# Kernel tuning notes

Hardware: AMD Instinct MI355X
Metric: run time of the kernel (lower is better)

## Reference

```python
import jax, jax.numpy as jnp
import numpy as np

B, S, D = 2, 2048, 1024
H = 16
HD = D // H  # head_dim = 64


def setup_inputs() -> dict:
    key = jax.random.key(0)
    ks = jax.random.split(key, 6)
    scale = 0.02
    x = jax.random.normal(ks[0], (B, S, D), dtype=jnp.float32)
    Wq = jax.random.normal(ks[1], (D, D), dtype=jnp.float32) * scale
    Wk = jax.random.normal(ks[2], (D, D), dtype=jnp.float32) * scale
    Wv = jax.random.normal(ks[3], (D, D), dtype=jnp.float32) * scale
    Wo = jax.random.normal(ks[4], (D, D), dtype=jnp.float32) * scale
    bo = jax.random.normal(ks[5], (D,), dtype=jnp.float32) * scale
    return {"x": x, "Wq": Wq, "Wk": Wk, "Wv": Wv, "Wo": Wo, "bo": bo}


def reference(x, Wq, Wk, Wv, Wo, bo):
    b, s, d = x.shape
    # QKV projections (no bias, qkv_bias=False)
    Q = (x @ Wq).reshape(b, s, H, HD)
    K = (x @ Wk).reshape(b, s, H, HD)
    V = (x @ Wv).reshape(b, s, H, HD)
    # [b, h, q, k] attention scores
    scores = jnp.einsum('bqhd,bkhd->bhqk', Q, K)
    # causal mask: positions k > q masked to -inf (applied before scaling, as in source;
    # -inf / sqrt(hd) is still -inf so this matches)
    causal = jnp.triu(jnp.ones((s, s), dtype=bool), k=1)
    scores = jnp.where(causal, -jnp.inf, scores)
    att = jax.nn.softmax(scores / jnp.sqrt(jnp.float32(HD)), axis=-1)
    # dropout p=0.0 -> identity
    ctx = jnp.einsum('bhqk,bkhd->bqhd', att, V).reshape(b, s, d)
    return ctx @ Wo + bo
```

## Files before the change

### kernel.cpp

```cpp
#include <hip/hip_runtime.h>

typedef __bf16 bf16;
typedef __attribute__((ext_vector_type(8))) __bf16 bf16x8;
typedef __attribute__((ext_vector_type(4))) __bf16 bf16x4;
typedef __attribute__((ext_vector_type(4))) float floatx4;

#define MFMA16(a, b, c) __builtin_amdgcn_mfma_f32_16x16x32_bf16((a), (b), (c), 0, 0, 0)

static constexpr int BB = 2, SS = 2048, DD = 1024, HH = 16;
static constexpr int MM = BB * SS;
static constexpr int N_QKV = 3 * DD;

__device__ __forceinline__ float exp2c(float x) {
#if __has_builtin(__builtin_amdgcn_exp2f)
    return __builtin_amdgcn_exp2f(x);
#else
    return exp2f(x);
#endif
}

__device__ __forceinline__ void async16(const void* g, void* l) {
    __builtin_amdgcn_global_load_lds(
        (const __attribute__((address_space(1))) unsigned int*)g,
        (__attribute__((address_space(3))) unsigned int*)l, 16, 0, 0);
}

__global__ __launch_bounds__(256) void prep_kernel(const float* __restrict__ x,
                                                   bf16* __restrict__ xb,
                                                   const float* __restrict__ w0,
                                                   const float* __restrict__ w1,
                                                   const float* __restrict__ w2,
                                                   const float* __restrict__ w3,
                                                   bf16* __restrict__ outT) {
    const int blk = blockIdx.x, tid = threadIdx.x;
    if (blk < 4096) {
        int i = blk * 1024 + tid * 4;
        float4 v = *(const float4*)(x + i);
        bf16x4 o;
        o[0] = (bf16)v.x; o[1] = (bf16)v.y; o[2] = (bf16)v.z; o[3] = (bf16)v.w;
        *(bf16x4*)(xb + i) = o;
    } else {
        __shared__ float tile[32][33];
        const int wblk = blk - 4096;
        const int z = wblk >> 10, rem = wblk & 1023;
        const int by = rem >> 5, bx = rem & 31;
        const float* src = (z == 0) ? w0 : (z == 1) ? w1 : (z == 2) ? w2 : w3;
        bf16* dst = outT + (size_t)z * DD * DD;
        const int y0 = by * 32, x0 = bx * 32;
        {
            const int tx = tid & 7, ty = tid >> 3;
            float4 v = *(const float4*)(src + (size_t)(y0 + ty) * DD + x0 + tx * 4);
            tile[ty][tx * 4 + 0] = v.x;
            tile[ty][tx * 4 + 1] = v.y;
            tile[ty][tx * 4 + 2] = v.z;
            tile[ty][tx * 4 + 3] = v.w;
        }
        __syncthreads();
        {
            const int tx = tid & 7, c = tid >> 3;
            bf16x4 o;
            o[0] = (bf16)tile[tx * 4 + 0][c];
            o[1] = (bf16)tile[tx * 4 + 1][c];
            o[2] = (bf16)tile[tx * 4 + 2][c];
            o[3] = (bf16)tile[tx * 4 + 3][c];
            *(bf16x4*)(dst + (size_t)(x0 + c) * DD + y0 + tx * 4) = o;
        }
    }
}

template <int BM, int BN, bool OUT_BF16>
__global__ __launch_bounds__(256) void gemm_kernel(const bf16* __restrict__ A,
                                                   const bf16* __restrict__ Bt,
                                                   void* __restrict__ C,
                                                   const float* __restrict__ bias,
                                                   int K, int ldc) {
    constexpr int MT = BM / 32, NT = BN / 32;
    __shared__ bf16 As[BM * 64];
    __shared__ bf16 Bs[BN * 64];
    const int tid = threadIdx.x, wave = tid >> 6, lane = tid & 63;
    const int quad = lane >> 4, l16 = lane & 15;
    const int wm = wave >> 1, wn = wave & 1;
    const int m0 = blockIdx.y * BM, n0 = blockIdx.x * BN;
    const int l8r = lane >> 3, l8c = lane & 7;
    const int gch = ((l8c ^ l8r) * 8);

    floatx4 acc[MT][NT] = {};

    for (int k0 = 0; k0 < K; k0 += 64) {
        __syncthreads();
#pragma unroll
        for (int c = 0; c < BM / 32; ++c) {
            int r = wave * (BM / 4) + c * 8;
            async16(A + (size_t)(m0 + r + l8r) * K + k0 + gch, &As[r * 64]);
        }
#pragma unroll
        for (int c = 0; c < BN / 32; ++c) {
            int r = wave * (BN / 4) + c * 8;
            async16(Bt + (size_t)(n0 + r + l8r) * K + k0 + gch, &Bs[r * 64]);
        }
        __syncthreads();
#pragma unroll
        for (int cc = 0; cc < 2; ++cc) {
            bf16x8 af[MT], bv[NT];
#pragma unroll
            for (int i = 0; i < MT; ++i) {
                int row = wm * (BM / 2) + i * 16 + l16;
                af[i] = *(const bf16x8*)&As[row * 64 + ((cc * 4 + quad) ^ (row & 7)) * 8];
            }
#pragma unroll
            for (int j = 0; j < NT; ++j) {
                int row = wn * (BN / 2) + j * 16 + l16;
                bv[j] = *(const bf16x8*)&Bs[row * 64 + ((cc * 4 + quad) ^ (row & 7)) * 8];
            }
#pragma unroll
            for (int i = 0; i < MT; ++i)
#pragma unroll
                for (int j = 0; j < NT; ++j)
                    acc[i][j] = MFMA16(af[i], bv[j], acc[i][j]);
        }
    }

#pragma unroll
    for (int i = 0; i < MT; ++i)
#pragma unroll
        for (int j = 0; j < NT; ++j)
#pragma unroll
            for (int r = 0; r < 4; ++r) {
                int row = m0 + wm * (BM / 2) + i * 16 + quad * 4 + r;
                int col = n0 + wn * (BN / 2) + j * 16 + l16;
                if (OUT_BF16)
                    ((bf16*)C)[(size_t)row * ldc + col] = (bf16)acc[i][j][r];
                else
                    ((float*)C)[(size_t)row * ldc + col] = acc[i][j][r] + bias[col];
            }
}

__global__ __launch_bounds__(512, 2) void gemm192_kernel(const bf16* __restrict__ A,
                                                         const bf16* __restrict__ Bt,
                                                         bf16* __restrict__ C,
                                                         bf16* __restrict__ Vt_g,
                                                         int K, int ldc) {
    __shared__ __align__(16) bf16 As[2 * 256 * 64];
    __shared__ __align__(16) bf16 Bs[2 * 192 * 64];
    const int tid = threadIdx.x, wave = tid >> 6, lane = tid & 63;
    const int quad = lane >> 4, l16 = lane & 15;
    const int wm = wave >> 2, wn = wave & 3;
    const int m0 = blockIdx.y * 256, n0 = blockIdx.x * 192;
    const int l8r = lane >> 3, l8c = lane & 7;
    const int gch = (l8c ^ l8r) * 8;
    const int nk = K >> 6;

    floatx4 acc[2][4][3] = {};
    bf16x8 af[4][2], bn[3][2];

#define VMW(N) asm volatile("s_waitcnt vmcnt(" #N ")" ::: "memory")
#define BARX __builtin_amdgcn_s_barrier()

#define STAGE_A(H, KN, BUF)                                                       \
    {                                                                             \
        _Pragma("unroll") for (int c = 0; c < 2; ++c) {                           \
            int r0 = (H) * 128 + c * 64 + wave * 8;                               \
            async16(A + (size_t)(m0 + r0 + l8r) * K + (KN) + gch,                 \
                    &As[(BUF) * 16384 + r0 * 64]);                                \
        }                                                                         \
    }
#define STAGE_B(KN, BUF)                                                          \
    {                                                                             \
        _Pragma("unroll") for (int c = 0; c < 3; ++c) {                           \
            int r0 = wave * 24 + c * 8;                                           \
            async16(Bt + (size_t)(n0 + r0 + l8r) * K + (KN) + gch,                \
                    &Bs[(BUF) * 12288 + r0 * 64]);                                \
        }                                                                         \
    }
#define READ_A(MH, BUF)                                                           \
    {                                                                             \
        _Pragma("unroll") for (int m = 0; m < 4; ++m) {                           \
            int row = (MH) * 128 + wm * 64 + m * 16 + l16;                        \
            _Pragma("unroll") for (int kk = 0; kk < 2; ++kk)                      \
                af[m][kk] = *(const bf16x8*)&As[(BUF) * 16384 + row * 64 +        \
                                               (((kk * 4 + quad) ^ (row & 7)) * 8)]; \
        }                                                                         \
    }
#define READ_B(BUF)                                                               \
    {                                                                             \
        _Pragma("unroll") for (int n = 0; n < 3; ++n) {                           \
            int row = wn * 48 + n * 16 + l16;                                     \
            _Pragma("unroll") for (int kk = 0; kk < 2; ++kk)                      \
                bn[n][kk] = *(const bf16x8*)&Bs[(BUF) * 12288 + row * 64 +        \
                                               (((kk * 4 + quad) ^ (row & 7)) * 8)]; \
        }                                                                         \
    }
#define MMAC(MH)                                                                  \
    {                                                                             \
        __builtin_amdgcn_s_setprio(1);                                            \
        _Pragma("unroll") for (int m = 0; m < 4; ++m)                             \
            _Pragma("unroll") for (int n = 0; n < 3; ++n)                         \
                _Pragma("unroll") for (int kk = 0; kk < 2; ++kk)                  \
                    acc[MH][m][n] = MFMA16(af[m][kk], bn[n][kk], acc[MH][m][n]);  \
        __builtin_amdgcn_s_setprio(0);                                            \
    }

    STAGE_A(0, 0, 0);
    STAGE_B(0, 0);
    STAGE_A(1, 0, 0);

    for (int kt = 0; kt < nk; ++kt) {
        const int buf = kt & 1;
        const int knext = (kt + 1) << 6;
        const bool last = (kt == nk - 1);

        VMW(2);
        BARX;
        READ_A(0, buf);
        READ_B(buf);
        if (!last) { STAGE_A(0, knext, buf ^ 1); STAGE_B(knext, buf ^ 1); }
        MMAC(0);

        if (!last) { VMW(5); } else { VMW(0); }
        BARX;
        READ_A(1, buf);
        if (!last) STAGE_A(1, knext, buf ^ 1);
        MMAC(1);
    }

#undef VMW
#undef BARX
#undef STAGE_A
#undef STAGE_B
#undef READ_A
#undef READ_B
#undef MMAC

#pragma unroll
    for (int mh = 0; mh < 2; ++mh)
#pragma unroll
        for (int m = 0; m < 4; ++m)
#pragma unroll
            for (int n = 0; n < 3; ++n) {
                int grow = m0 + mh * 128 + wm * 64 + m * 16 + quad * 4;
                int gcol0 = n0 + wn * 48 + n * 16;
                if (gcol0 >= 2048) {
                    int bb = grow >> 11, s = grow & (SS - 1);
                    int vcol = gcol0 + l16 - 2048;
                    int hh = vcol >> 6, hd = vcol & 63;
                    bf16x4 pk;
#pragma unroll
                    for (int r = 0; r < 4; ++r) pk[r] = (bf16)acc[mh][m][n][r];
                    *(bf16x4*)&Vt_g[(((size_t)(bb * 16 + hh)) * 64 + hd) * SS + s] = pk;
                } else {
#pragma unroll
                    for (int r = 0; r < 4; ++r)
                        C[(size_t)(grow + r) * ldc + gcol0 + l16] = (bf16)acc[mh][m][n][r];
                }
            }
}

__global__ __launch_bounds__(256, 4) void attn_kernel(const bf16* __restrict__ QKV,
                                                      const bf16* __restrict__ Vt_g,
                                                      bf16* __restrict__ ctx) {
    __shared__ __align__(16) bf16 smem[20480];
    bf16* Ks = smem;
    bf16* Vt = smem + 8192;
    bf16* Ps = smem + 16384;
    bf16* Qs = Ps;

    const int tid = threadIdx.x, wave = tid >> 6, lane = tid & 63;
    const int quad = lane >> 4, l16 = lane & 15;
    const int gb = blockIdx.x;
    const int xcd = gb & 7, rr = gb >> 3;
    const int hi = rr >> 5, lo = rr & 31;
    const int t = (hi == 0) ? lo : (hi == 1) ? (31 - lo)
                : (hi == 2) ? (lo ^ 16) : (31 - (lo ^ 16));
    const int bh = xcd * 4 + hi;
    const int b = bh >> 4, h = bh & 15;
    const int q0 = t * 64;
    const size_t base = (size_t)(b * SS) * N_QKV;
    const bf16* Vg = Vt_g + (size_t)bh * 64 * SS;
    constexpr float C2 = 0.18033688011112042f;
    const int l8r = lane >> 3, l8c = lane & 7;
    const int gch = (l8c ^ l8r) * 8;
    const int swz = l16 & 7;
    const int nkt = t + 1;

    {
#pragma unroll
        for (int c = 0; c < 2; ++c) {
            int r0 = wave * 16 + c * 8;
            async16(QKV + base + (size_t)(q0 + r0 + l8r) * N_QKV + h * 64 + gch,
                    Qs + r0 * 64);
            async16(QKV + base + (size_t)(r0 + l8r) * N_QKV + DD + h * 64 + gch,
                    Ks + r0 * 64);
            async16(Vg + (size_t)(r0 + l8r) * SS + gch, Vt + r0 * 64);
        }
    }
    __syncthreads();

    bf16x8 qf[2];
#pragma unroll
    for (int cc = 0; cc < 2; ++cc) {
        int row = wave * 16 + l16;
        qf[cc] = *(const bf16x8*)&Qs[row * 64 + ((cc * 4 + quad) ^ swz) * 8];
    }

    bf16x8 onesf = {};
    if (l16 == 0) {
#pragma unroll
        for (int e = 0; e < 8; ++e) onesf[e] = (bf16)1.0f;
    }

    floatx4 accv[4] = {};
    floatx4 acc5 = {};
    const int qg = q0 + wave * 16 + l16;

    for (int kt = 0; kt < nkt; ++kt) {
        const int buf = kt & 1;
        if (kt + 1 < nkt) {
            const int k0n = (kt + 1) * 64;
            const int dst = (buf ^ 1) * 4096;
#pragma unroll
            for (int c = 0; c < 2; ++c) {
                int r0 = wave * 16 + c * 8;
                async16(QKV + base + (size_t)(k0n + r0 + l8r) * N_QKV + DD + h * 64 + gch,
                        Ks + dst + r0 * 64);
                async16(Vg + (size_t)(r0 + l8r) * SS + k0n + gch, Vt + dst + r0 * 64);
            }
        }
        const int k0 = kt * 64;

        floatx4 st[4];
#pragma unroll
        for (int j = 0; j < 4; ++j) st[j] = (floatx4){};
        __builtin_amdgcn_s_setprio(1);
#pragma unroll
        for (int cc = 0; cc < 2; ++cc)
#pragma unroll
            for (int j = 0; j < 4; ++j) {
                bf16x8 kf = *(const bf16x8*)&Ks[buf * 4096 + (j * 16 + l16) * 64
                                                + ((cc * 4 + quad) ^ swz) * 8];
                st[j] = MFMA16(kf, qf[cc], st[j]);
            }
        __builtin_amdgcn_s_setprio(0);

        if (kt == nkt - 1) {
#pragma unroll
            for (int j = 0; j < 4; ++j) {
                int kb = k0 + j * 16 + quad * 4;
#pragma unroll
                for (int r = 0; r < 4; ++r)
                    if (kb + r > qg) st[j][r] = -__builtin_inff();
            }
        }

#pragma unroll
        for (int j = 0; j < 4; ++j) {
            bf16x4 pk4;
#pragma unroll
            for (int r = 0; r < 4; ++r)
                pk4[r] = (bf16)exp2c(st[j][r] * C2);
            *(bf16x4*)&Ps[wave * 1024 + l16 * 64
                          + ((2 * j + (quad >> 1)) ^ swz) * 8 + (quad & 1) * 4] = pk4;
        }

        bf16x8 pf[2];
#pragma unroll
        for (int cc = 0; cc < 2; ++cc)
            pf[cc] = *(const bf16x8*)&Ps[wave * 1024 + l16 * 64
                                         + ((cc * 4 + quad) ^ swz) * 8];
        __builtin_amdgcn_s_setprio(1);
#pragma unroll
        for (int cc = 0; cc < 2; ++cc)
#pragma unroll
            for (int j = 0; j < 4; ++j) {
                bf16x8 vt = *(const bf16x8*)&Vt[buf * 4096 + (j * 16 + l16) * 64
                                                + ((cc * 4 + quad) ^ swz) * 8];
                accv[j] = MFMA16(pf[cc], vt, accv[j]);
            }
        acc5 = MFMA16(pf[0], onesf, acc5);
        acc5 = MFMA16(pf[1], onesf, acc5);
        __builtin_amdgcn_s_setprio(0);

        __syncthreads();
    }

    float inv[4];
#pragma unroll
    for (int r = 0; r < 4; ++r)
        inv[r] = 1.0f / __shfl(acc5[r], lane & 48, 64);
#pragma unroll
    for (int j = 0; j < 4; ++j)
#pragma unroll
        for (int r = 0; r < 4; ++r) {
            int row = b * SS + q0 + wave * 16 + quad * 4 + r;
            int col = h * 64 + j * 16 + l16;
            ctx[(size_t)row * DD + col] = (bf16)(accv[j][r] * inv[r]);
        }
}

extern "C" void kernel_launch(void* const* d_in, const int* in_sizes, int n_in,
                              void* d_out, int out_size, void* d_ws, size_t ws_size,
                              hipStream_t stream) {
    const float* x  = (const float*)d_in[0];
    const float* Wq = (const float*)d_in[1];
    const float* Wk = (const float*)d_in[2];
    const float* Wv = (const float*)d_in[3];
    const float* Wo = (const float*)d_in[4];
    const float* bo = (const float*)d_in[5];
    float* out = (float*)d_out;

    char* ws = (char*)d_ws;
    bf16* xb   = (bf16*)ws;
    bf16* WT   = (bf16*)(ws + (size_t)(8  << 20));
    bf16* QKV  = (bf16*)(ws + (size_t)(16 << 20));
    bf16* ctxb = (bf16*)(ws + (size_t)(40 << 20));
    bf16* Vt_g = (bf16*)(ws + (size_t)(48 << 20));

    prep_kernel<<<dim3(8192), dim3(256), 0, stream>>>(x, xb, Wq, Wk, Wv, Wo, WT);
    gemm192_kernel<<<dim3(N_QKV / 192, MM / 256), dim3(512), 0, stream>>>(
        xb, WT, QKV, Vt_g, DD, N_QKV);
    attn_kernel<<<dim3(1024), dim3(256), 0, stream>>>(QKV, Vt_g, ctxb);
    gemm_kernel<128, 64, false><<<dim3(DD / 64, MM / 128), dim3(256), 0, stream>>>(
        ctxb, WT + (size_t)3 * DD * DD, out, bo, DD, DD);
}
```

Baseline: 162.8 us.

## Replace output projection GEMM with double-buffered pipelined 128x128 kernel

Swaps the simple single-buffered output projection GEMM for a 512-thread, 128x128-tile kernel. It double-buffers LDS with async global-to-LDS loads, splits each k-step into two halves with partial vmcnt waits, and raises priority around the MFMA blocks. This reuses the pipelining scheme from the QKV GEMM and aims to overlap loads with MFMA work and cut per-iteration barrier stalls. The grid drops to 256 blocks, which may leave some CUs underused.

```diff
diff --git a/kernel.cpp b/kernel.cpp
--- a/kernel.cpp
+++ b/kernel.cpp
@@ -68,73 +68,6 @@
     }
 }
 
-template <int BM, int BN, bool OUT_BF16>
-__global__ __launch_bounds__(256) void gemm_kernel(const bf16* __restrict__ A,
-                                                   const bf16* __restrict__ Bt,
-                                                   void* __restrict__ C,
-                                                   const float* __restrict__ bias,
-                                                   int K, int ldc) {
-    constexpr int MT = BM / 32, NT = BN / 32;
-    __shared__ bf16 As[BM * 64];
-    __shared__ bf16 Bs[BN * 64];
-    const int tid = threadIdx.x, wave = tid >> 6, lane = tid & 63;
-    const int quad = lane >> 4, l16 = lane & 15;
-    const int wm = wave >> 1, wn = wave & 1;
-    const int m0 = blockIdx.y * BM, n0 = blockIdx.x * BN;
-    const int l8r = lane >> 3, l8c = lane & 7;
-    const int gch = ((l8c ^ l8r) * 8);
-
-    floatx4 acc[MT][NT] = {};
-
-    for (int k0 = 0; k0 < K; k0 += 64) {
-        __syncthreads();
-#pragma unroll
-        for (int c = 0; c < BM / 32; ++c) {
-            int r = wave * (BM / 4) + c * 8;
-            async16(A + (size_t)(m0 + r + l8r) * K + k0 + gch, &As[r * 64]);
-        }
-#pragma unroll
-        for (int c = 0; c < BN / 32; ++c) {
-            int r = wave * (BN / 4) + c * 8;
-            async16(Bt + (size_t)(n0 + r + l8r) * K + k0 + gch, &Bs[r * 64]);
-        }
-        __syncthreads();
-#pragma unroll
-        for (int cc = 0; cc < 2; ++cc) {
-            bf16x8 af[MT], bv[NT];
-#pragma unroll
-            for (int i = 0; i < MT; ++i) {
-                int row = wm * (BM / 2) + i * 16 + l16;
-                af[i] = *(const bf16x8*)&As[row * 64 + ((cc * 4 + quad) ^ (row & 7)) * 8];
-            }
-#pragma unroll
-            for (int j = 0; j < NT; ++j) {
-                int row = wn * (BN / 2) + j * 16 + l16;
-                bv[j] = *(const bf16x8*)&Bs[row * 64 + ((cc * 4 + quad) ^ (row & 7)) * 8];
-            }
-#pragma unroll
-            for (int i = 0; i < MT; ++i)
-#pragma unroll
-                for (int j = 0; j < NT; ++j)
-                    acc[i][j] = MFMA16(af[i], bv[j], acc[i][j]);
-        }
-    }
-
-#pragma unroll
-    for (int i = 0; i < MT; ++i)
-#pragma unroll
-        for (int j = 0; j < NT; ++j)
-#pragma unroll
-            for (int r = 0; r < 4; ++r) {
-                int row = m0 + wm * (BM / 2) + i * 16 + quad * 4 + r;
-                int col = n0 + wn * (BN / 2) + j * 16 + l16;
-                if (OUT_BF16)
-                    ((bf16*)C)[(size_t)row * ldc + col] = (bf16)acc[i][j][r];
-                else
-                    ((float*)C)[(size_t)row * ldc + col] = acc[i][j][r] + bias[col];
-            }
-}
-
 __global__ __launch_bounds__(512, 2) void gemm192_kernel(const bf16* __restrict__ A,
                                                          const bf16* __restrict__ Bt,
                                                          bf16* __restrict__ C,
@@ -223,8 +156,6 @@
         MMAC(1);
     }
 
-#undef VMW
-#undef BARX
 #undef STAGE_A
 #undef STAGE_B
 #undef READ_A
@@ -253,6 +184,111 @@
                         C[(size_t)(grow + r) * ldc + gcol0 + l16] = (bf16)acc[mh][m][n][r];
                 }
             }
+}
+
+__global__ __launch_bounds__(512, 2) void gemmo_kernel(const bf16* __restrict__ A,
+                                                       const bf16* __restrict__ Bt,
+                                                       float* __restrict__ C,
+                                                       const float* __restrict__ bias,
+                                                       int K, int ldc) {
+    __shared__ __align__(16) bf16 As[2 * 128 * 64];
+    __shared__ __align__(16) bf16 Bs[2 * 128 * 64];
+    const int tid = threadIdx.x, wave = tid >> 6, lane = tid & 63;
+    const int quad = lane >> 4, l16 = lane & 15;
+    const int wm = wave >> 2, wn = wave & 3;
+    const int m0 = blockIdx.y * 128, n0 = blockIdx.x * 128;
+    const int l8r = lane >> 3, l8c = lane & 7;
+    const int gch = (l8c ^ l8r) * 8;
+    const int nk = K >> 6;
+
+    floatx4 acc[2][2][2] = {};
+    bf16x8 af[2][2], bn[2][2];
+
+#define STAGE_A(H, KN, BUF)                                                       \
+    {                                                                             \
+        int r0 = (H) * 64 + wave * 8;                                             \
+        async16(A + (size_t)(m0 + r0 + l8r) * K + (KN) + gch,                     \
+                &As[(BUF) * 8192 + r0 * 64]);                                     \
+    }
+#define STAGE_B(KN, BUF)                                                          \
+    {                                                                             \
+        _Pragma("unroll") for (int c = 0; c < 2; ++c) {                           \
+            int r0 = wave * 16 + c * 8;                                           \
+            async16(Bt + (size_t)(n0 + r0 + l8r) * K + (KN) + gch,                \
+                    &Bs[(BUF) * 8192 + r0 * 64]);                                 \
+        }                                                                         \
+    }
+#define READ_A(MH, BUF)                                                           \
+    {                                                                             \
+        _Pragma("unroll") for (int m = 0; m < 2; ++m) {                           \
+            int row = (MH) * 64 + wm * 32 + m * 16 + l16;                         \
+            _Pragma("unroll") for (int kk = 0; kk < 2; ++kk)                      \
+                af[m][kk] = *(const bf16x8*)&As[(BUF) * 8192 + row * 64 +         \
+                                               (((kk * 4 + quad) ^ (row & 7)) * 8)]; \
+        }                                                                         \
+    }
+#define READ_B(BUF)                                                               \
+    {                                                                             \
+        _Pragma("unroll") for (int n = 0; n < 2; ++n) {                           \
+            int row = wn * 32 + n * 16 + l16;                                     \
+            _Pragma("unroll") for (int kk = 0; kk < 2; ++kk)                      \
+                bn[n][kk] = *(const bf16x8*)&Bs[(BUF) * 8192 + row * 64 +         \
+                                               (((kk * 4 + quad) ^ (row & 7)) * 8)]; \
+        }                                                                         \
+    }
+#define MMAC(MH)                                                                  \
+    {                                                                             \
+        __builtin_amdgcn_s_setprio(1);                                            \
+        _Pragma("unroll") for (int m = 0; m < 2; ++m)                             \
+            _Pragma("unroll") for (int n = 0; n < 2; ++n)                         \
+                _Pragma("unroll") for (int kk = 0; kk < 2; ++kk)                  \
+                    acc[MH][m][n] = MFMA16(af[m][kk], bn[n][kk], acc[MH][m][n]);  \
+        __builtin_amdgcn_s_setprio(0);                                            \
+    }
+
+    STAGE_A(0, 0, 0);
+    STAGE_B(0, 0);
+    STAGE_A(1, 0, 0);
+
+    for (int kt = 0; kt < nk; ++kt) {
+        const int buf = kt & 1;
+        const int knext = (kt + 1) << 6;
+        const bool last = (kt == nk - 1);
+
+        VMW(1);
+        BARX;
+        READ_A(0, buf);
+        READ_B(buf);
+        if (!last) { STAGE_A(0, knext, buf ^ 1); STAGE_B(knext, buf ^ 1); }
+        MMAC(0);
+
+        if (!last) { VMW(3); } else { VMW(0); }
+        BARX;
+        READ_A(1, buf);
+        if (!last) STAGE_A(1, knext, buf ^ 1);
+        MMAC(1);
+    }
+
+#undef VMW
+#undef BARX
+#undef STAGE_A
+#undef STAGE_B
+#undef READ_A
+#undef READ_B
+#undef MMAC
+
+#pragma unroll
+    for (int mh = 0; mh < 2; ++mh)
+#pragma unroll
+        for (int m = 0; m < 2; ++m)
+#pragma unroll
+            for (int n = 0; n < 2; ++n)
+#pragma unroll
+                for (int r = 0; r < 4; ++r) {
+                    int row = m0 + mh * 64 + wm * 32 + m * 16 + quad * 4 + r;
+                    int col = n0 + wn * 32 + n * 16 + l16;
+                    C[(size_t)row * ldc + col] = acc[mh][m][n][r] + bias[col];
+                }
 }
 
 __global__ __launch_bounds__(256, 4) void attn_kernel(const bf16* __restrict__ QKV,
@@ -418,6 +454,6 @@
     gemm192_kernel<<<dim3(N_QKV / 192, MM / 256), dim3(512), 0, stream>>>(
         xb, WT, QKV, Vt_g, DD, N_QKV);
     attn_kernel<<<dim3(1024), dim3(256), 0, stream>>>(QKV, Vt_g, ctxb);
-    gemm_kernel<128, 64, false><<<dim3(DD / 64, MM / 128), dim3(256), 0, stream>>>(
+    gemmo_kernel<<<dim3(DD / 128, MM / 128), dim3(512), 0, stream>>>(
         ctxb, WT + (size_t)3 * DD * DD, out, bo, DD, DD);
 }
```

Result: no change. 164.2 us (+0.9%).
